# Optimization experiments

Hardware: AMD Instinct MI355X
Metric: run time of the kernel (lower is better)

## Reference

```python
import jax, jax.numpy as jnp
from jax import lax
import numpy as np

EPS = 1e-5
K = 3


def _conv(x, w, b, pad, dil=1, groups=1):
    out = lax.conv_general_dilated(
        x, w, (1, 1), [(pad, pad), (pad, pad)], rhs_dilation=(dil, dil),
        dimension_numbers=('NCHW', 'OIHW', 'NCHW'), feature_group_count=groups)
    return out + b[None, :, None, None]


def _bn(x, g, b, m, v):
    scale = g / jnp.sqrt(v + EPS)
    return (x - m[None, :, None, None]) * scale[None, :, None, None] + b[None, :, None, None]


def setup_inputs() -> dict:
    key = jax.random.key(0)
    ks = jax.random.split(key, 24)
    B, C, H, W = 8, 256, 48, 80
    Hd = 256  # hidden_channels
    n = lambda k, s, sc=0.05: (jax.random.normal(k, s, dtype=jnp.float32) * sc)
    return {
        'f_t_minus_2': jax.random.normal(ks[0], (B, C, H, W), dtype=jnp.float32),
        'f_t_minus_1': jax.random.normal(ks[1], (B, C, H, W), dtype=jnp.float32),
        'f_t':         jax.random.normal(ks[2], (B, C, H, W), dtype=jnp.float32),
        'ov_w1': n(ks[3], (Hd, 3 * C, 3, 3)), 'ov_b1': n(ks[4], (Hd,)),
        'bn1_g': jnp.ones((Hd,), jnp.float32), 'bn1_b': jnp.zeros((Hd,), jnp.float32),
        'bn1_m': n(ks[5], (Hd,)), 'bn1_v': jax.random.uniform(ks[6], (Hd,), jnp.float32, 0.5, 1.5),
        'ov_w2': n(ks[7], (Hd, Hd, 3, 3)), 'ov_b2': n(ks[8], (Hd,)),
        'bn2_g': jnp.ones((Hd,), jnp.float32), 'bn2_b': jnp.zeros((Hd,), jnp.float32),
        'bn2_m': n(ks[9], (Hd,)), 'bn2_v': jax.random.uniform(ks[10], (Hd,), jnp.float32, 0.5, 1.5),
        'g_w': n(ks[11], (C, Hd, 1, 1)), 'g_b': n(ks[12], (C,)),
        'fc1_w': n(ks[13], (512, 2 * C)), 'fc1_b': n(ks[14], (512,)),
        'fc2_w': n(ks[15], (C * K * K, 512)), 'fc2_b': n(ks[16], (C * K * K,)),
        'ap_w': n(ks[17], (1, 2 * C, 1, 1)), 'ap_b': n(ks[18], (1,)),
        'a_w': n(ks[19], (1, 2 * C, 1, 1)), 'a_b': jnp.ones((1,), jnp.float32),
    }


def reference(f_t_minus_2, f_t_minus_1, f_t,
              ov_w1, ov_b1, bn1_g, bn1_b, bn1_m, bn1_v,
              ov_w2, ov_b2, bn2_g, bn2_b, bn2_m, bn2_v,
              g_w, g_b, fc1_w, fc1_b, fc2_w, fc2_b,
              ap_w, ap_b, a_w, a_b):
    B, C, H, W = f_t.shape
    # (1) Overview-Net (GCM)
    f_concat = jnp.concatenate([f_t_minus_2, f_t_minus_1, f_t], axis=1)
    h = jax.nn.relu(_bn(_conv(f_concat, ov_w1, ov_b1, pad=2, dil=2), bn1_g, bn1_b, bn1_m, bn1_v))
    h = jax.nn.relu(_bn(_conv(h, ov_w2, ov_b2, pad=4, dil=4), bn2_g, bn2_b, bn2_m, bn2_v))
    g_pooled = h.mean(axis=(2, 3), keepdims=True)            # [B,Hd,1,1]
    G = _conv(g_pooled, g_w, g_b, pad=0)                     # [B,C,1,1]
    # (2) Focus-Net: FC-generated per-(batch,channel) 3x3 depthwise conv on (f_t, f_{t-1})
    Fs = jnp.concatenate([f_t, f_t_minus_1], axis=0)         # [2B,C,H,W]
    g_flat = jnp.repeat(G.reshape(B, C), 2, axis=0)          # [2B,C]
    gap = Fs.mean(axis=(2, 3))                               # [2B,C]
    fc_in = jnp.concatenate([g_flat, gap], axis=1)           # [2B,2C]
    w = jax.nn.silu(fc_in @ fc1_w.T + fc1_b) @ fc2_w.T + fc2_b  # [2B, C*9]
    w = w.reshape(2 * B * C, 1, K, K)
    x = Fs.reshape(1, 2 * B * C, H, W)
    out = lax.conv_general_dilated(
        x, w, (1, 1), [(1, 1), (1, 1)],
        dimension_numbers=('NCHW', 'OIHW', 'NCHW'), feature_group_count=2 * B * C)
    out = out.reshape(2 * B, C, H, W)
    f_t_mod, f_t1_mod = out[:B], out[B:]
    # (3) Dynamic fusion
    f_prev_cat = jnp.concatenate([f_t1_mod, f_t_minus_2], axis=1)
    alpha_prev = 0.3 + 0.4 * jax.nn.sigmoid(_conv(f_prev_cat, ap_w, ap_b, pad=0))
    f_prev = alpha_prev * f_t1_mod + (1.0 - alpha_prev) * f_t_minus_2
    f_cat = jnp.concatenate([f_t_mod, f_prev], axis=1)
    alpha = 0.6 + 0.3 * jax.nn.sigmoid(_conv(f_cat, a_w, a_b, pad=0))
    return alpha * f_t_mod + (1.0 - alpha) * f_prev
```

## Files before the change

kernel.cpp:

```cpp
#include <hip/hip_runtime.h>
#include <hip/hip_bf16.h>
#include <math.h>


typedef __bf16 bf16x8 __attribute__((ext_vector_type(8)));
typedef float f32x4 __attribute__((ext_vector_type(4)));
typedef __attribute__((address_space(1))) void as1_void;
typedef __attribute__((address_space(3))) void as3_void;


__global__ __launch_bounds__(256) void prep_consts_kernel(
    const float* __restrict__ ob1, const float* __restrict__ g1, const float* __restrict__ b1,
    const float* __restrict__ m1, const float* __restrict__ v1,
    const float* __restrict__ ob2, const float* __restrict__ g2, const float* __restrict__ b2,
    const float* __restrict__ m2, const float* __restrict__ v2,
    float* __restrict__ cst)
{
  int i = threadIdx.x;
  float a1 = g1[i] / sqrtf(v1[i] + 1e-5f);
  cst[i]       = a1;
  cst[256 + i] = (ob1[i] - m1[i]) * a1 + b1[i];
  float a2 = g2[i] / sqrtf(v2[i] + 1e-5f);
  cst[512 + i] = a2;
  cst[768 + i] = (ob2[i] - m2[i]) * a2 + b2[i];
}

__global__ __launch_bounds__(256) void pad_concat_kernel(
    const float* __restrict__ f2, const float* __restrict__ f1, const float* __restrict__ f0,
    __hip_bfloat16* __restrict__ out, float* __restrict__ gapv)
{
  int bid = blockIdx.x;
  const int cg = bid % 6; bid /= 6;
  const int y = bid % 48;
  const int b = bid / 48;

  __shared__ float tile[128 * 85];

  const float* src = (cg < 2) ? f2 : ((cg < 4) ? f1 : f0);
  const int ccbase = (cg & 1) * 128;
  const uint4 z4 = {0u, 0u, 0u, 0u};

#pragma unroll
  for (int it = 0; it < 10; it++) {
    const int idx = it * 256 + threadIdx.x;
    const int cl = idx / 20, x4 = idx % 20;
    const float4 v = *(const float4*)(src +
        (((size_t)b * 256 + ccbase + cl) * 48 + y) * 80 + x4 * 4);
    float* t = tile + cl * 85 + x4 * 4;
    t[0] = v.x; t[1] = v.y; t[2] = v.z; t[3] = v.w;
  }

  if (threadIdx.x < 32) {
    const int xb_ = threadIdx.x >> 3, ch8 = threadIdx.x & 7;
    const int xx = (xb_ < 2) ? xb_ : (80 + xb_);
    *(uint4*)(out + ((size_t)(b * 52 + y + 2) * 84 + xx) * 768 + cg * 128 + ch8 * 8) = z4;
  }
  if (y == 0 || y == 47) {
    const int r0 = (y == 0) ? 0 : 50;
    for (int idx = threadIdx.x; idx < 1344; idx += 256) {
      const int rr = idx / 672, rem = idx % 672;
      const int xx = rem >> 3, ch8 = rem & 7;
      *(uint4*)(out + ((size_t)(b * 52 + r0 + rr) * 84 + xx) * 768 + cg * 128 + ch8 * 8) = z4;
    }
  }
  __syncthreads();

  __hip_bfloat16* obase = out + ((size_t)(b * 52 + y + 2) * 84 + 2) * 768 + cg * 128;
#pragma unroll
  for (int it = 0; it < 5; it++) {
    const int idx = it * 256 + threadIdx.x;
    const int chunk = idx & 15, x = idx >> 4;
    const float* t = tile + chunk * 8 * 85 + x;
    union { __hip_bfloat16 h[8]; uint4 u; } pk;
#pragma unroll
    for (int j = 0; j < 8; j++) pk.h[j] = __float2bfloat16(t[j * 85]);
    *(uint4*)(obase + (size_t)x * 768 + chunk * 8) = pk.u;
  }

  if (cg >= 2) {
    const int i_gap = (cg >= 4) ? b : (b + 8);
    const int cl = threadIdx.x >> 1, half = threadIdx.x & 1;
    const float* t = tile + cl * 85 + half * 40;
    float s = 0.f;
#pragma unroll
    for (int k = 0; k < 40; k++) s += t[k];
    s += __shfl_xor(s, 1);
    if (half == 0) atomicAdd(&gapv[i_gap * 256 + ccbase + cl], s);
  }
}

__global__ __launch_bounds__(256) void repack_w_kernel(
    const float* __restrict__ w, __hip_bfloat16* __restrict__ out, int OC, int IC)
{
  int idx = blockIdx.x * 256 + threadIdx.x;
  if (idx >= OC * IC * 9) return;
  int ic = idx % IC;
  int t = idx / IC;
  int oc = t % OC;
  int tap = t / OC;
  out[idx] = __float2bfloat16(w[(oc * IC + ic) * 9 + tap]);
}

template <int CIN, int HP, int WP, int DIL, int MODE>
__global__ __launch_bounds__(256) void conv_mfma_kernel(
    const __hip_bfloat16* __restrict__ inp, const __hip_bfloat16* __restrict__ wt,
    const float* __restrict__ bnA, const float* __restrict__ bnB,
    __hip_bfloat16* __restrict__ outp, float* __restrict__ gpool)
{
  __shared__ unsigned short As[8192] __attribute__((aligned(16)));
  __shared__ unsigned short Bs[8192] __attribute__((aligned(16)));

  int bid = blockIdx.x;
  bid = (bid & 7) * 60 + (bid >> 3);
  const int ocb = bid & 1; bid >>= 1;
  const int xb = bid % 5; bid /= 5;
  const int yb = bid % 6; bid /= 6;
  const int b = bid;
  const int y0 = yb * 8, x0 = xb * 16, oc0 = ocb * 128;

  const int t = threadIdx.x;
  const int w = t >> 6, l = t & 63;
  const int col16 = l & 15, quad = l >> 4;
  const int wm = w >> 1, wn = w & 1;
  const int rsub = l >> 3;
  const int jj = (l & 7) ^ rsub;

  f32x4 acc[4][4];
  const f32x4 zf = {0.f, 0.f, 0.f, 0.f};
#pragma unroll
  for (int i = 0; i < 4; i++)
#pragma unroll
    for (int j = 0; j < 4; j++) acc[i][j] = zf;

  for (int c0 = 0; c0 < CIN; c0 += 64) {
    for (int tap = 0; tap < 9; tap++) {
      const int ty = tap / 3, tx = tap - ty * 3;
      const __hip_bfloat16* inBase =
          inp + ((size_t)(b * HP + y0 + DIL * ty) * WP + (x0 + DIL * tx)) * CIN + jj * 8 + c0;
      const __hip_bfloat16* wBase = wt + (size_t)(tap * 256 + oc0) * CIN + jj * 8 + c0;
      __syncthreads();
#pragma unroll
      for (int i = 0; i < 4; i++) {
        const int q = i * 4 + w;
        const int m = q * 8 + rsub;
        const int ry = m >> 4, rx = m & 15;
        const __hip_bfloat16* gp = inBase + (ry * WP + rx) * CIN;
        __builtin_amdgcn_global_load_lds((as1_void*)gp,
            (as3_void*)((char*)As + q * 1024), 16, 0, 0);
      }
#pragma unroll
      for (int i = 0; i < 4; i++) {
        const int q = i * 4 + w;
        const int n = q * 8 + rsub;
        const __hip_bfloat16* gp = wBase + n * CIN;
        __builtin_amdgcn_global_load_lds((as1_void*)gp,
            (as3_void*)((char*)Bs + q * 1024), 16, 0, 0);
      }
      __syncthreads();
#pragma unroll
      for (int kiter = 0; kiter < 2; kiter++) {
        bf16x8 af[4], bg[4];
#pragma unroll
        for (int fi = 0; fi < 4; fi++) {
          const int m = wm * 64 + fi * 16 + col16;
          const int jc = (kiter * 4 + quad) ^ (m & 7);
          af[fi] = *(const bf16x8*)((const char*)As + m * 128 + jc * 16);
        }
#pragma unroll
        for (int fi = 0; fi < 4; fi++) {
          const int n = wn * 64 + fi * 16 + col16;
          const int jc = (kiter * 4 + quad) ^ (n & 7);
          bg[fi] = *(const bf16x8*)((const char*)Bs + n * 128 + jc * 16);
        }
#pragma unroll
        for (int fm_ = 0; fm_ < 4; fm_++)
#pragma unroll
          for (int fn_ = 0; fn_ < 4; fn_++)
            acc[fm_][fn_] = __builtin_amdgcn_mfma_f32_16x16x32_bf16(
                af[fm_], bg[fn_], acc[fm_][fn_], 0, 0, 0);
      }
    }
  }

  if (MODE == 0) {
#pragma unroll
    for (int fn_ = 0; fn_ < 4; fn_++) {
      const int oc = oc0 + wn * 64 + fn_ * 16 + col16;
      const float sa = bnA[oc], sb = bnB[oc];
#pragma unroll
      for (int fm_ = 0; fm_ < 4; fm_++) {
#pragma unroll
        for (int r = 0; r < 4; r++) {
          const int m = wm * 64 + fm_ * 16 + quad * 4 + r;
          const int y = y0 + (m >> 4), x = x0 + (m & 15);
          const float v = fmaxf(acc[fm_][fn_][r] * sa + sb, 0.f);
          outp[((size_t)(b * 56 + y + 4) * 88 + (x + 4)) * 256 + oc] = __float2bfloat16(v);
        }
      }
    }
  } else {
#pragma unroll
    for (int fn_ = 0; fn_ < 4; fn_++) {
      const int oc = oc0 + wn * 64 + fn_ * 16 + col16;
      const float sa = bnA[oc], sb = bnB[oc];
      float cs = 0.f;
#pragma unroll
      for (int fm_ = 0; fm_ < 4; fm_++)
#pragma unroll
        for (int r = 0; r < 4; r++)
          cs += fmaxf(acc[fm_][fn_][r] * sa + sb, 0.f);
      cs += __shfl_xor(cs, 16);
      cs += __shfl_xor(cs, 32);
      if (quad == 0) atomicAdd(&gpool[b * 256 + oc], cs);
    }
  }
}


__global__ __launch_bounds__(256) void fcG_kernel(
    const float* __restrict__ gpool, const float* __restrict__ gw,
    const float* __restrict__ gb, float* __restrict__ G)
{
  int b = blockIdx.x, oc = threadIdx.x;
  __shared__ float pool[256];
  pool[oc] = gpool[b * 256 + oc] * (1.f / 3840.f);
  __syncthreads();
  float s = gb[oc];
  const float* wr = gw + oc * 256;
  for (int c2 = 0; c2 < 256; c2++) s += pool[c2] * wr[c2];
  G[b * 256 + oc] = s;
}

__global__ __launch_bounds__(256) void fc1_kernel(
    const float* __restrict__ G, const float* __restrict__ gapv,
    const float* __restrict__ w, const float* __restrict__ bias,
    float* __restrict__ out1)
{
  __shared__ float fin[16][513];
  for (int idx = threadIdx.x; idx < 16 * 512; idx += 256) {
    int i = idx >> 9, k = idx & 511;
    fin[i][k] = (k < 256) ? G[(i >> 1) * 256 + k]
                          : gapv[i * 256 + (k - 256)] * (1.f / 3840.f);
  }
  __syncthreads();
  int g = blockIdx.x * 256 + threadIdx.x;
  int j = g >> 4, i = g & 15;
  float s = bias[j];
  const float* wr = w + j * 512;
  for (int k = 0; k < 512; k++) s += fin[i][k] * wr[k];
  out1[j * 16 + i] = s / (1.f + expf(-s));
}

__global__ __launch_bounds__(256) void fc2_kernel(
    const float* __restrict__ out1, const float* __restrict__ w,
    const float* __restrict__ bias, float* __restrict__ wdw)
{
  __shared__ float fin[16][513];
  for (int idx = threadIdx.x; idx < 16 * 512; idx += 256) {
    int i = idx >> 9, k = idx & 511;
    fin[i][k] = out1[k * 16 + i];
  }
  __syncthreads();
  int g = blockIdx.x * 256 + threadIdx.x;
  int j = g >> 4, i = g & 15;
  float s = bias[j];
  const float* wr = w + j * 512;
  for (int k = 0; k < 512; k++) s += fin[i][k] * wr[k];
  wdw[i * 2304 + j] = s;
}

__global__ __launch_bounds__(256) void dw_kernel(
    const float* __restrict__ f0, const float* __restrict__ f1,
    const float* __restrict__ wdw, float* __restrict__ fm)
{
  int i = blockIdx.x >> 8, c = blockIdx.x & 255;
  const float* src = (i < 8) ? (f0 + ((size_t)i * 256 + c) * 3840)
                             : (f1 + ((size_t)(i - 8) * 256 + c) * 3840);
  float* dst = fm + ((size_t)i * 256 + c) * 3840;
  __shared__ float w9s[9];
  __shared__ float tile[50][82];
  for (int k = threadIdx.x; k < 4100; k += 256) ((float*)tile)[k] = 0.f;
  if (threadIdx.x < 9) w9s[threadIdx.x] = wdw[i * 2304 + c * 9 + threadIdx.x];
  __syncthreads();
  for (int k = threadIdx.x; k < 960; k += 256) {
    const float4 v = *(const float4*)(src + k * 4);
    const int y = k / 20, xx = (k % 20) * 4;
    float* tp = &tile[y + 1][xx + 1];
    tp[0] = v.x; tp[1] = v.y; tp[2] = v.z; tp[3] = v.w;
  }
  __syncthreads();
  for (int k = threadIdx.x; k < 960; k += 256) {
    const int y = k / 20, xx = (k % 20) * 4;
    float r0 = 0.f, r1 = 0.f, r2 = 0.f, r3 = 0.f;
#pragma unroll
    for (int dy = 0; dy < 3; dy++) {
      const float* row = &tile[y + dy][xx];
      const float w0 = w9s[dy * 3], w1 = w9s[dy * 3 + 1], w2 = w9s[dy * 3 + 2];
      r0 += w0 * row[0] + w1 * row[1] + w2 * row[2];
      r1 += w0 * row[1] + w1 * row[2] + w2 * row[3];
      r2 += w0 * row[2] + w1 * row[3] + w2 * row[4];
      r3 += w0 * row[3] + w1 * row[4] + w2 * row[5];
    }
    float4 o; o.x = r0; o.y = r1; o.z = r2; o.w = r3;
    *(float4*)(dst + k * 4) = o;
  }
}

__global__ __launch_bounds__(640) void alpha_final_kernel(
    const float* __restrict__ fm, const float* __restrict__ f2,
    const float* __restrict__ apw, const float* __restrict__ apb,
    const float* __restrict__ aw, const float* __restrict__ ab,
    float* __restrict__ out)
{
  int b = blockIdx.x / 48, y = blockIdx.x % 48;
  int x = threadIdx.x % 80, g = threadIdx.x / 80;
  const float* ftm  = fm + ((size_t)(b * 256) + g * 32) * 3840 + y * 80 + x;
  const float* ft1m = fm + ((size_t)((b + 8) * 256) + g * 32) * 3840 + y * 80 + x;
  const float* ptm2 = f2 + ((size_t)(b * 256) + g * 32) * 3840 + y * 80 + x;

  float v0[32], v1[32], v2[32];
  float S = 0.f, T0 = 0.f, T1 = 0.f, T2 = 0.f;
#pragma unroll
  for (int cc = 0; cc < 32; cc++) {
    v0[cc] = ftm[(size_t)cc * 3840];
    v1[cc] = ft1m[(size_t)cc * 3840];
    v2[cc] = ptm2[(size_t)cc * 3840];
    const int c = g * 32 + cc;
    S  += apw[c] * v1[cc] + apw[256 + c] * v2[cc];
    T0 += aw[c] * v0[cc];
    T1 += aw[256 + c] * v1[cc];
    T2 += aw[256 + c] * v2[cc];
  }
  __shared__ float red[4][8][80];
  __shared__ float apl[80], alb[80];
  red[0][g][x] = S; red[1][g][x] = T0; red[2][g][x] = T1; red[3][g][x] = T2;
  __syncthreads();
  if (g == 0) {
    float s = 0.f, t0 = 0.f, t1 = 0.f, t2 = 0.f;
#pragma unroll
    for (int k = 0; k < 8; k++) {
      s += red[0][k][x]; t0 += red[1][k][x]; t1 += red[2][k][x]; t2 += red[3][k][x];
    }
    float ap = 0.3f + 0.4f / (1.f + expf(-(s + apb[0])));
    float A  = t0 + ap * t1 + (1.f - ap) * t2 + ab[0];
    float al = 0.6f + 0.3f / (1.f + expf(-A));
    apl[x] = ap; alb[x] = al;
  }
  __syncthreads();
  const float ap = apl[x], al = alb[x];
  float* ob = out + ((size_t)(b * 256) + g * 32) * 3840 + y * 80 + x;
#pragma unroll
  for (int cc = 0; cc < 32; cc++)
    ob[(size_t)cc * 3840] = al * v0[cc] + (1.f - al) * (ap * v1[cc] + (1.f - ap) * v2[cc]);
}


extern "C" void kernel_launch(void* const* d_in, const int* in_sizes, int n_in,
                              void* d_out, int out_size, void* d_ws, size_t ws_size,
                              hipStream_t stream)
{
  const float* f_tm2 = (const float*)d_in[0];
  const float* f_tm1 = (const float*)d_in[1];
  const float* f_t   = (const float*)d_in[2];
  const float* ov_w1 = (const float*)d_in[3];
  const float* ov_b1 = (const float*)d_in[4];
  const float* bn1_g = (const float*)d_in[5];
  const float* bn1_b = (const float*)d_in[6];
  const float* bn1_m = (const float*)d_in[7];
  const float* bn1_v = (const float*)d_in[8];
  const float* ov_w2 = (const float*)d_in[9];
  const float* ov_b2 = (const float*)d_in[10];
  const float* bn2_g = (const float*)d_in[11];
  const float* bn2_b = (const float*)d_in[12];
  const float* bn2_m = (const float*)d_in[13];
  const float* bn2_v = (const float*)d_in[14];
  const float* g_w   = (const float*)d_in[15];
  const float* g_b   = (const float*)d_in[16];
  const float* fc1_w = (const float*)d_in[17];
  const float* fc1_b = (const float*)d_in[18];
  const float* fc2_w = (const float*)d_in[19];
  const float* fc2_b = (const float*)d_in[20];
  const float* ap_w  = (const float*)d_in[21];
  const float* ap_b  = (const float*)d_in[22];
  const float* a_w   = (const float*)d_in[23];
  const float* a_b   = (const float*)d_in[24];

  char* ws = (char*)d_ws;
  float* fm            = (float*)ws;
  __hip_bfloat16* in1p = (__hip_bfloat16*)ws;
  __hip_bfloat16* wt1  = (__hip_bfloat16*)(ws + 53673984);
  __hip_bfloat16* wt2  = (__hip_bfloat16*)(ws + 57212928);
  __hip_bfloat16* h1p  = (__hip_bfloat16*)(ws + 58392576);
  float* gpool         = (float*)(ws + 78577664);
  float* gapv          = (float*)(ws + 78585856);
  float* Gv            = (float*)(ws + 78602240);
  float* out1          = (float*)(ws + 78610432);
  float* wdw           = (float*)(ws + 78643200);
  float* cst           = (float*)(ws + 79036416);

  hipMemsetAsync(h1p, 0, 20185088, stream);
  hipMemsetAsync(gpool, 0, 24576, stream);

  prep_consts_kernel<<<1, 256, 0, stream>>>(ov_b1, bn1_g, bn1_b, bn1_m, bn1_v,
                                            ov_b2, bn2_g, bn2_b, bn2_m, bn2_v, cst);
  pad_concat_kernel<<<2304, 256, 0, stream>>>(f_tm2, f_tm1, f_t, in1p, gapv);
  repack_w_kernel<<<6912, 256, 0, stream>>>(ov_w1, wt1, 256, 768);
  repack_w_kernel<<<2304, 256, 0, stream>>>(ov_w2, wt2, 256, 256);

  conv_mfma_kernel<768, 52, 84, 2, 0><<<480, 256, 0, stream>>>(in1p, wt1, cst, cst + 256, h1p, nullptr);
  conv_mfma_kernel<256, 56, 88, 4, 1><<<480, 256, 0, stream>>>(h1p, wt2, cst + 512, cst + 768, nullptr, gpool);

  fcG_kernel<<<8, 256, 0, stream>>>(gpool, g_w, g_b, Gv);
  fc1_kernel<<<32, 256, 0, stream>>>(Gv, gapv, fc1_w, fc1_b, out1);
  fc2_kernel<<<144, 256, 0, stream>>>(out1, fc2_w, fc2_b, wdw);
  dw_kernel<<<4096, 256, 0, stream>>>(f_t, f_tm1, wdw, fm);
  alpha_final_kernel<<<384, 640, 0, stream>>>(fm, f_tm2, ap_w, ap_b, a_w, a_b, (float*)d_out);
}
```

Before: 458.3 us.

## Split-K the first conv across three blocks and coalesce weight repacking

The first 768-channel conv now splits its input-channel loop into three slices, so 1440 blocks run instead of 480. Each slice writes fp32 partial sums to a workspace buffer, and a new reduce kernel adds them and applies BN+ReLU before writing padded bf16 output. The aim is better CU occupancy on MI355X, since 480 blocks underfill 256 CUs. The cost is roughly 94 MB of extra fp32 writes plus reads and one more kernel launch. The weight repack kernel is also rewritten to stage each 128-channel slice in LDS and emit vectorized 16-byte stores, where it previously used scattered scalar writes.

```diff
diff --git a/kernel.cpp b/kernel.cpp
--- a/kernel.cpp
+++ b/kernel.cpp
@@ -92,13 +92,21 @@
 __global__ __launch_bounds__(256) void repack_w_kernel(
     const float* __restrict__ w, __hip_bfloat16* __restrict__ out, int OC, int IC)
 {
-  int idx = blockIdx.x * 256 + threadIdx.x;
-  if (idx >= OC * IC * 9) return;
-  int ic = idx % IC;
-  int t = idx / IC;
-  int oc = t % OC;
-  int tap = t / OC;
-  out[idx] = __float2bfloat16(w[(oc * IC + ic) * 9 + tap]);
+  const int nicb = IC >> 7;
+  const int icb = blockIdx.x % nicb;
+  const int oc  = blockIdx.x / nicb;
+  const int ic0 = icb * 128;
+  __shared__ float wl[1152];
+  const float* src = w + ((size_t)oc * IC + ic0) * 9;
+  for (int k = threadIdx.x; k < 1152; k += 256) wl[k] = src[k];
+  __syncthreads();
+  if (threadIdx.x < 144) {
+    const int tap = threadIdx.x / 16, ch = threadIdx.x % 16;
+    union { __hip_bfloat16 h[8]; uint4 u; } pk;
+#pragma unroll
+    for (int j = 0; j < 8; j++) pk.h[j] = __float2bfloat16(wl[(ch * 8 + j) * 9 + tap]);
+    *(uint4*)(out + ((size_t)tap * OC + oc) * IC + ic0 + ch * 8) = pk.u;
+  }
 }
 
 template <int CIN, int HP, int WP, int DIL, int MODE>
@@ -111,7 +119,13 @@
   __shared__ unsigned short Bs[8192] __attribute__((aligned(16)));
 
   int bid = blockIdx.x;
-  bid = (bid & 7) * 60 + (bid >> 3);
+  int kc = 0;
+  if (MODE == 2) {
+    bid = (bid & 7) * 180 + (bid >> 3);
+    kc = bid % 3; bid /= 3;
+  } else {
+    bid = (bid & 7) * 60 + (bid >> 3);
+  }
   const int ocb = bid & 1; bid >>= 1;
   const int xb = bid % 5; bid /= 5;
   const int yb = bid % 6; bid /= 6;
@@ -132,7 +146,9 @@
 #pragma unroll
     for (int j = 0; j < 4; j++) acc[i][j] = zf;
 
-  for (int c0 = 0; c0 < CIN; c0 += 64) {
+  const int cbeg = (MODE == 2) ? kc * (CIN / 3) : 0;
+  const int cend = (MODE == 2) ? cbeg + CIN / 3 : CIN;
+  for (int c0 = cbeg; c0 < cend; c0 += 64) {
     for (int tap = 0; tap < 9; tap++) {
       const int ty = tap / 3, tx = tap - ty * 3;
       const __hip_bfloat16* inBase =
@@ -198,7 +214,7 @@
         }
       }
     }
-  } else {
+  } else if (MODE == 1) {
 #pragma unroll
     for (int fn_ = 0; fn_ < 4; fn_++) {
       const int oc = oc0 + wn * 64 + fn_ * 16 + col16;
@@ -213,7 +229,44 @@
       cs += __shfl_xor(cs, 32);
       if (quad == 0) atomicAdd(&gpool[b * 256 + oc], cs);
     }
-  }
+  } else {
+    float* pb = gpool + (size_t)kc * 7864320;
+#pragma unroll
+    for (int fn_ = 0; fn_ < 4; fn_++) {
+      const int oc = oc0 + wn * 64 + fn_ * 16 + col16;
+#pragma unroll
+      for (int fm_ = 0; fm_ < 4; fm_++) {
+#pragma unroll
+        for (int r = 0; r < 4; r++) {
+          const int m = wm * 64 + fm_ * 16 + quad * 4 + r;
+          const int y = y0 + (m >> 4), x = x0 + (m & 15);
+          const int p = (b * 48 + y) * 80 + x;
+          pb[(size_t)p * 256 + oc] = acc[fm_][fn_][r];
+        }
+      }
+    }
+  }
+}
+
+__global__ __launch_bounds__(256) void reduce_split_kernel(
+    const float* __restrict__ pbuf, const float* __restrict__ bnA,
+    const float* __restrict__ bnB, __hip_bfloat16* __restrict__ outp)
+{
+  const size_t i4 = ((size_t)blockIdx.x * 256 + threadIdx.x) * 4;
+  const float4 a = *(const float4*)(pbuf + i4);
+  const float4 bq = *(const float4*)(pbuf + 7864320 + i4);
+  const float4 c = *(const float4*)(pbuf + 2 * 7864320 + i4);
+  const int oc = (int)(i4 & 255);
+  const int p  = (int)(i4 >> 8);
+  const int b = p / 3840, rem = p % 3840, y = rem / 80, x = rem % 80;
+  const float4 sa = *(const float4*)(bnA + oc);
+  const float4 sb = *(const float4*)(bnB + oc);
+  union { __hip_bfloat16 h[4]; uint2 u; } pk;
+  pk.h[0] = __float2bfloat16(fmaxf((a.x + bq.x + c.x) * sa.x + sb.x, 0.f));
+  pk.h[1] = __float2bfloat16(fmaxf((a.y + bq.y + c.y) * sa.y + sb.y, 0.f));
+  pk.h[2] = __float2bfloat16(fmaxf((a.z + bq.z + c.z) * sa.z + sb.z, 0.f));
+  pk.h[3] = __float2bfloat16(fmaxf((a.w + bq.w + c.w) * sa.w + sb.w, 0.f));
+  *(uint2*)(outp + ((size_t)(b * 56 + y + 4) * 88 + (x + 4)) * 256 + oc) = pk.u;
 }
 
 
@@ -397,6 +450,9 @@
   float* out1          = (float*)(ws + 78610432);
   float* wdw           = (float*)(ws + 78643200);
   float* cst           = (float*)(ws + 79036416);
+  float* pbuf          = (float*)(ws + 79040512);
+
+  const bool doSplit = (ws_size >= (size_t)79040512 + 3u * 31457280u);
 
   hipMemsetAsync(h1p, 0, 20185088, stream);
   hipMemsetAsync(gpool, 0, 24576, stream);
@@ -404,10 +460,15 @@
   prep_consts_kernel<<<1, 256, 0, stream>>>(ov_b1, bn1_g, bn1_b, bn1_m, bn1_v,
                                             ov_b2, bn2_g, bn2_b, bn2_m, bn2_v, cst);
   pad_concat_kernel<<<2304, 256, 0, stream>>>(f_tm2, f_tm1, f_t, in1p, gapv);
-  repack_w_kernel<<<6912, 256, 0, stream>>>(ov_w1, wt1, 256, 768);
-  repack_w_kernel<<<2304, 256, 0, stream>>>(ov_w2, wt2, 256, 256);
-
-  conv_mfma_kernel<768, 52, 84, 2, 0><<<480, 256, 0, stream>>>(in1p, wt1, cst, cst + 256, h1p, nullptr);
+  repack_w_kernel<<<1536, 256, 0, stream>>>(ov_w1, wt1, 256, 768);
+  repack_w_kernel<<<512, 256, 0, stream>>>(ov_w2, wt2, 256, 256);
+
+  if (doSplit) {
+    conv_mfma_kernel<768, 52, 84, 2, 2><<<1440, 256, 0, stream>>>(in1p, wt1, cst, cst + 256, nullptr, pbuf);
+    reduce_split_kernel<<<7680, 256, 0, stream>>>(pbuf, cst, cst + 256, h1p);
+  } else {
+    conv_mfma_kernel<768, 52, 84, 2, 0><<<480, 256, 0, stream>>>(in1p, wt1, cst, cst + 256, h1p, nullptr);
+  }
   conv_mfma_kernel<256, 56, 88, 4, 1><<<480, 256, 0, stream>>>(h1p, wt2, cst + 512, cst + 768, nullptr, gpool);
 
   fcG_kernel<<<8, 256, 0, stream>>>(gpool, g_w, g_b, Gv);
```

New measurement: 481.5 us. +5.1%, slower.

## Fuse weight repack, border-only zeroing and BN constants into one aux kernel

Applied to the files above, without the earlier changes.

Replaces the two memsets, the constant-prep kernel and two weight repack kernels with a single multi-role kernel. Weight repacking now stages 128-channel slices in shared memory and writes packed 16-byte bf16 vectors instead of scalar strided reads and writes. The full 20 MB memset of the padded hidden buffer is replaced by zeroing only the halo border, relying on conv1 to write every interior pixel. This cuts launch count and memory traffic, but is only correct if the interior is always fully overwritten.

```diff
diff --git a/kernel.cpp b/kernel.cpp
--- a/kernel.cpp
+++ b/kernel.cpp
@@ -8,21 +8,57 @@
 typedef __attribute__((address_space(1))) void as1_void;
 typedef __attribute__((address_space(3))) void as3_void;
 
-
-__global__ __launch_bounds__(256) void prep_consts_kernel(
+__global__ __launch_bounds__(256) void aux_kernel(
+    const float* __restrict__ w1, const float* __restrict__ w2,
     const float* __restrict__ ob1, const float* __restrict__ g1, const float* __restrict__ b1,
     const float* __restrict__ m1, const float* __restrict__ v1,
     const float* __restrict__ ob2, const float* __restrict__ g2, const float* __restrict__ b2,
     const float* __restrict__ m2, const float* __restrict__ v2,
+    __hip_bfloat16* __restrict__ wt1, __hip_bfloat16* __restrict__ wt2,
+    __hip_bfloat16* __restrict__ h1p, float* __restrict__ gzero,
     float* __restrict__ cst)
 {
-  int i = threadIdx.x;
-  float a1 = g1[i] / sqrtf(v1[i] + 1e-5f);
-  cst[i]       = a1;
-  cst[256 + i] = (ob1[i] - m1[i]) * a1 + b1[i];
-  float a2 = g2[i] / sqrtf(v2[i] + 1e-5f);
-  cst[512 + i] = a2;
-  cst[768 + i] = (ob2[i] - m2[i]) * a2 + b2[i];
+  __shared__ float wl[1152];
+  const int bid = blockIdx.x;
+  const uint4 z4 = {0u, 0u, 0u, 0u};
+
+  if (bid < 2048) {
+    const float* w = (bid < 1536) ? w1 : w2;
+    __hip_bfloat16* out = (bid < 1536) ? wt1 : wt2;
+    const int IC = (bid < 1536) ? 768 : 256;
+    const int lb = (bid < 1536) ? bid : (bid - 1536);
+    const int nicb = IC >> 7;
+    const int icb = lb % nicb, oc = lb / nicb;
+    const int ic0 = icb * 128;
+    const float* src = w + ((size_t)oc * IC + ic0) * 9;
+    for (int k = threadIdx.x; k < 1152; k += 256) wl[k] = src[k];
+    __syncthreads();
+    if (threadIdx.x < 144) {
+      const int tap = threadIdx.x / 16, ch = threadIdx.x % 16;
+      union { __hip_bfloat16 h[8]; uint4 u; } pk;
+#pragma unroll
+      for (int j = 0; j < 8; j++) pk.h[j] = __float2bfloat16(wl[(ch * 8 + j) * 9 + tap]);
+      *(uint4*)(out + ((size_t)tap * 256 + oc) * IC + ic0 + ch * 8) = pk.u;
+    }
+  } else if (bid < 3136) {
+    const int s = (bid - 2048) * 256 + threadIdx.x;
+    const int px = s >> 5, ch8 = s & 31;
+    const int b = px / 1088, r = px % 1088;
+    int y, x;
+    if (r < 704) { const int yi = r / 88; y = (yi < 4) ? yi : 48 + yi; x = r % 88; }
+    else { const int r2 = r - 704; y = 4 + (r2 >> 3); const int xi = r2 & 7; x = (xi < 4) ? xi : 80 + xi; }
+    *(uint4*)(h1p + ((size_t)(b * 56 + y) * 88 + x) * 256 + ch8 * 8) = z4;
+  } else if (bid < 3142) {
+    ((uint4*)gzero)[(bid - 3136) * 256 + threadIdx.x] = z4;
+  } else {
+    const int i = threadIdx.x;
+    float a1 = g1[i] / sqrtf(v1[i] + 1e-5f);
+    cst[i]       = a1;
+    cst[256 + i] = (ob1[i] - m1[i]) * a1 + b1[i];
+    float a2 = g2[i] / sqrtf(v2[i] + 1e-5f);
+    cst[512 + i] = a2;
+    cst[768 + i] = (ob2[i] - m2[i]) * a2 + b2[i];
+  }
 }
 
 __global__ __launch_bounds__(256) void pad_concat_kernel(
@@ -87,18 +123,6 @@
     s += __shfl_xor(s, 1);
     if (half == 0) atomicAdd(&gapv[i_gap * 256 + ccbase + cl], s);
   }
-}
-
-__global__ __launch_bounds__(256) void repack_w_kernel(
-    const float* __restrict__ w, __hip_bfloat16* __restrict__ out, int OC, int IC)
-{
-  int idx = blockIdx.x * 256 + threadIdx.x;
-  if (idx >= OC * IC * 9) return;
-  int ic = idx % IC;
-  int t = idx / IC;
-  int oc = t % OC;
-  int tap = t / OC;
-  out[idx] = __float2bfloat16(w[(oc * IC + ic) * 9 + tap]);
 }
 
 template <int CIN, int HP, int WP, int DIL, int MODE>
@@ -398,14 +422,10 @@
   float* wdw           = (float*)(ws + 78643200);
   float* cst           = (float*)(ws + 79036416);
 
-  hipMemsetAsync(h1p, 0, 20185088, stream);
-  hipMemsetAsync(gpool, 0, 24576, stream);
-
-  prep_consts_kernel<<<1, 256, 0, stream>>>(ov_b1, bn1_g, bn1_b, bn1_m, bn1_v,
-                                            ov_b2, bn2_g, bn2_b, bn2_m, bn2_v, cst);
+  aux_kernel<<<3143, 256, 0, stream>>>(ov_w1, ov_w2,
+      ov_b1, bn1_g, bn1_b, bn1_m, bn1_v, ov_b2, bn2_g, bn2_b, bn2_m, bn2_v,
+      wt1, wt2, h1p, gpool, cst);
   pad_concat_kernel<<<2304, 256, 0, stream>>>(f_tm2, f_tm1, f_t, in1p, gapv);
-  repack_w_kernel<<<6912, 256, 0, stream>>>(ov_w1, wt1, 256, 768);
-  repack_w_kernel<<<2304, 256, 0, stream>>>(ov_w2, wt2, 256, 256);
 
   conv_mfma_kernel<768, 52, 84, 2, 0><<<480, 256, 0, stream>>>(in1p, wt1, cst, cst + 256, h1p, nullptr);
   conv_mfma_kernel<256, 56, 88, 4, 1><<<480, 256, 0, stream>>>(h1p, wt2, cst + 512, cst + 768, nullptr, gpool);
```

Result: faster. 444.6 us (-3.0%).
